# Kernel optimization log

Hardware: AMD Instinct MI355X
Metric: run time of the kernel (lower is better)

## Reference

```python
import jax, jax.numpy as jnp
import numpy as np
from math import comb

K = 10            # Bernstein polynomial order
N = 100000        # num nodes
E = 3200000       # num edges


def _bern_prop(x, row, col, temp):
    """BernNet propagation: sum_k relu(temp)_k * C(K,k)/2^K * L^k (2I-L)^{K-k} x,
    with L = I - D^{-1/2} A D^{-1/2} built from the directed edge list."""
    theta = jax.nn.relu(temp)
    deg = jax.ops.segment_sum(jnp.ones((row.shape[0],), dtype=x.dtype), row, num_segments=N)
    dinv = jnp.where(deg > 0, jax.lax.rsqrt(deg), jnp.zeros_like(deg))
    w = (dinv[row] * dinv[col])[:, None]  # normalized adjacency edge weights [E,1]

    def adj(v):  # A_hat @ v : gather-multiply-scatter over edges
        return jax.ops.segment_sum(v[col] * w, row, num_segments=N)

    # tmp[i] = (2I - L)^i x = (I + A_hat)^i x
    tmp = [x]
    v = x
    for _ in range(K):
        v = v + adj(v)
        tmp.append(v)

    scale = 1.0 / (2 ** K)
    out = (comb(K, 0) * scale) * theta[0] * tmp[K]
    for i in range(K):
        v = tmp[K - i - 1]
        for _ in range(i + 1):  # apply L = I - A_hat, (i+1) times
            v = v - adj(v)
        out = out + (comb(K, i + 1) * scale) * theta[i + 1] * v
    return out


def setup_inputs() -> dict:
    key = jax.random.key(0)
    ks = jax.random.split(key, 5)
    x = jax.random.normal(ks[0], (N, 512), dtype=jnp.float32)
    edge_index = jax.random.randint(ks[1], (2, E), 0, N, dtype=jnp.int32)
    W1 = jax.random.normal(ks[2], (512, 256), dtype=jnp.float32) * 0.04
    b1 = jnp.zeros((256,), jnp.float32)
    W2 = jax.random.normal(ks[3], (256, 64), dtype=jnp.float32) * 0.06
    b2 = jnp.zeros((64,), jnp.float32)
    temp = jnp.ones((K + 1,), jnp.float32)  # Bern_prop param, initialized to ones
    return {"x": x, "edge_index": edge_index, "W1": W1, "b1": b1, "W2": W2, "b2": b2, "temp": temp}


def reference(x, edge_index, W1, b1, W2, b2, temp):
    # eval mode: dropout is identity; self.m (BatchNorm) is never called in forward
    row, col = edge_index[0], edge_index[1]
    h = jax.nn.relu(x @ W1 + b1)   # lin1 + relu
    h = h @ W2 + b2                # lin2 -> [N, num_classes]
    h = _bern_prop(h, row, col, temp)
    return jax.nn.log_softmax(h, axis=1)
```

## Files before the change

kernel.cpp:

```cpp
#include <hip/hip_runtime.h>
#include <hip/hip_bf16.h>

#define K_ORDER 10
#define NNODES  100000
#define NEDGES  3200000

typedef __bf16 bf16x8 __attribute__((ext_vector_type(8)));
typedef float  floatx4 __attribute__((ext_vector_type(4)));

struct WS {
  float* d;
  int*   jmax;
  int*   cnt;
  int*   off;
  int*   cursor;
  float* dinv;
  int*   csr_col;
  float* csr_w;
  short* h1;
  float* h2;
  float* buf0;
  float* buf1;
  short* w1s;
  short* w2s;
};

__device__ inline short f2bf(float f) {
  __hip_bfloat16 h = __float2bfloat16(f);
  return __builtin_bit_cast(short, h);
}

__global__ void k_coeff(const float* __restrict__ temp, WS ws) {
  if (threadIdx.x != 0) return;
  const double C10[11] = {1,10,45,120,210,252,210,120,45,10,1};
  double dd[11];
  for (int j = 0; j <= K_ORDER; ++j) dd[j] = 0.0;
  for (int k = 0; k <= K_ORDER; ++k) {
    double th = temp[k] > 0.f ? (double)temp[k] : 0.0;
    double c  = th * C10[k] / 1024.0;
    double p[11];
    for (int j = 0; j <= K_ORDER; ++j) p[j] = 0.0;
    p[0] = 1.0;
    int deg = 0;
    for (int i = 0; i < K_ORDER - k; ++i) {
      ++deg;
      for (int j = deg; j >= 1; --j) p[j] += p[j-1];
    }
    for (int i = 0; i < k; ++i) {
      ++deg;
      for (int j = deg; j >= 1; --j) p[j] = p[j] - p[j-1];
    }
    for (int j = 0; j <= K_ORDER; ++j) dd[j] += c * p[j];
  }
  int jm = 0;
  for (int j = 1; j <= K_ORDER; ++j) if (dd[j] != 0.0) jm = j;
  for (int j = 0; j <= K_ORDER; ++j) ws.d[j] = (float)dd[j];
  *ws.jmax = jm;
}

__global__ void k_swz(const float* __restrict__ W, short* __restrict__ dst,
                      int Kd, int Nd) {
  int t = blockIdx.x * blockDim.x + threadIdx.x;
  int total = (Kd >> 5) * (Nd >> 4) * 64;
  if (t >= total) return;
  int lane = t & 63, frag = t >> 6;
  int nfr = Nd >> 4;
  int kt = frag / nfr, nc = frag - kt * nfr;
  int m16 = lane & 15, q = lane >> 4;
  int kbase = kt * 32 + q * 8;
  int col = nc * 16 + m16;
  short v[8];
#pragma unroll
  for (int j = 0; j < 8; ++j) v[j] = f2bf(W[(size_t)(kbase + j) * Nd + col]);
  short4* o = (short4*)&dst[(size_t)t * 8];
  o[0] = make_short4(v[0], v[1], v[2], v[3]);
  o[1] = make_short4(v[4], v[5], v[6], v[7]);
}

__global__ __launch_bounds__(256) void k_gemm1(const float* __restrict__ A,
    const short* __restrict__ Bsw, const float* __restrict__ bias,
    short* __restrict__ H1)
{
  __shared__ short As[4 * 64 * 8];
  const int tid = threadIdx.x;
  const int wave = tid >> 6, lane = tid & 63;
  const int q = lane >> 4, m16 = lane & 15;
  const int bm = blockIdx.x * 64;

  const int srow = tid >> 2, kq = tid & 3;
  const int r_ = srow >> 4, m_ = srow & 15;
  int grow = bm + srow; if (grow > NNODES - 1) grow = NNODES - 1;
  const float* aptr = A + (size_t)grow * 512 + kq * 8;
  short* sdst = &As[r_ * 512 + (kq * 16 + m_) * 8];

  float4 p0 = *(const float4*)(aptr);
  float4 p1 = *(const float4*)(aptr + 4);

  floatx4 acc[4][4] = {};

#pragma unroll 1
  for (int kt = 0; kt < 16; ++kt) {
    __syncthreads();
    ((short4*)sdst)[0] = make_short4(f2bf(p0.x), f2bf(p0.y), f2bf(p0.z), f2bf(p0.w));
    ((short4*)sdst)[1] = make_short4(f2bf(p1.x), f2bf(p1.y), f2bf(p1.z), f2bf(p1.w));
    __syncthreads();
    if (kt < 15) {
      p0 = *(const float4*)(aptr + (kt + 1) * 32);
      p1 = *(const float4*)(aptr + (kt + 1) * 32 + 4);
    }
    const short* bbase = Bsw + ((size_t)(kt * 16 + wave * 4) * 64 + lane) * 8;
    bf16x8 bf[4];
#pragma unroll
    for (int c = 0; c < 4; ++c) bf[c] = *(const bf16x8*)(bbase + c * 512);
    bf16x8 af[4];
#pragma unroll
    for (int r = 0; r < 4; ++r) af[r] = *(const bf16x8*)&As[r * 512 + lane * 8];
#pragma unroll
    for (int r = 0; r < 4; ++r)
#pragma unroll
      for (int c = 0; c < 4; ++c)
        acc[r][c] = __builtin_amdgcn_mfma_f32_16x16x32_bf16(af[r], bf[c], acc[r][c], 0, 0, 0);
  }

  float bv[4];
#pragma unroll
  for (int c = 0; c < 4; ++c) bv[c] = bias[wave * 64 + c * 16 + m16];
#pragma unroll
  for (int r = 0; r < 4; ++r) {
    int rb = bm + r * 16 + q * 4;
#pragma unroll
    for (int reg = 0; reg < 4; ++reg) {
      int rowm = rb + reg;
      if (rowm < NNODES) {
        size_t o = (size_t)rowm * 256 + wave * 64 + m16;
#pragma unroll
        for (int c = 0; c < 4; ++c)
          H1[o + c * 16] = f2bf(fmaxf(acc[r][c][reg] + bv[c], 0.f));
      }
    }
  }
}

__global__ __launch_bounds__(256) void k_gemm2(const short* __restrict__ H1,
    const short* __restrict__ B2sw, const float* __restrict__ bias,
    WS ws, float* __restrict__ out)
{
  const int tid = threadIdx.x;
  const int wave = tid >> 6, lane = tid & 63;
  const int q = lane >> 4, m16 = lane & 15;
  const int bm = blockIdx.x * 64;
  int grow = bm + wave * 16 + m16; if (grow > NNODES - 1) grow = NNODES - 1;
  const short* arow = H1 + (size_t)grow * 256 + q * 8;

  floatx4 acc[4] = {};
#pragma unroll
  for (int kt = 0; kt < 8; ++kt) {
    bf16x8 af = *(const bf16x8*)(arow + kt * 32);
    const short* bbase = B2sw + ((size_t)(kt * 4) * 64 + lane) * 8;
#pragma unroll
    for (int c = 0; c < 4; ++c) {
      bf16x8 bf = *(const bf16x8*)(bbase + c * 512);
      acc[c] = __builtin_amdgcn_mfma_f32_16x16x32_bf16(af, bf, acc[c], 0, 0, 0);
    }
  }

  int jm = *ws.jmax;
  float d0 = ws.d[0];
  float bv[4];
#pragma unroll
  for (int c = 0; c < 4; ++c) bv[c] = bias[c * 16 + m16];

  if (jm > 0) {
#pragma unroll
    for (int reg = 0; reg < 4; ++reg) {
      int rowm = bm + wave * 16 + q * 4 + reg;
      if (rowm < NNODES) {
        size_t o = (size_t)rowm * 64 + m16;
#pragma unroll
        for (int c = 0; c < 4; ++c)
          ws.h2[o + c * 16] = acc[c][reg] + bv[c];
      }
    }
  } else {
#pragma unroll
    for (int reg = 0; reg < 4; ++reg) {
      float v[4];
#pragma unroll
      for (int c = 0; c < 4; ++c) v[c] = d0 * (acc[c][reg] + bv[c]);
      float m = fmaxf(fmaxf(v[0], v[1]), fmaxf(v[2], v[3]));
#pragma unroll
      for (int o = 1; o < 16; o <<= 1) m = fmaxf(m, __shfl_xor(m, o));
      float s = 0.f;
#pragma unroll
      for (int c = 0; c < 4; ++c) s += __expf(v[c] - m);
#pragma unroll
      for (int o = 1; o < 16; o <<= 1) s += __shfl_xor(s, o);
      float ls = __logf(s);
      int rowm = bm + wave * 16 + q * 4 + reg;
      if (rowm < NNODES) {
        size_t o = (size_t)rowm * 64 + m16;
#pragma unroll
        for (int c = 0; c < 4; ++c) out[o + c * 16] = v[c] - m - ls;
      }
    }
  }
}

__global__ void k_zero(WS ws) {
  if (*ws.jmax == 0) return;
  int stride = gridDim.x * blockDim.x;
  for (int i = blockIdx.x * blockDim.x + threadIdx.x; i < NNODES; i += stride) {
    ws.cnt[i] = 0; ws.cursor[i] = 0;
  }
}

__global__ void k_count(const int* __restrict__ ei, WS ws) {
  if (*ws.jmax == 0) return;
  int stride = gridDim.x * blockDim.x;
  for (int e = blockIdx.x * blockDim.x + threadIdx.x; e < NEDGES; e += stride)
    atomicAdd(&ws.cnt[ei[e]], 1);
}

__global__ __launch_bounds__(1024) void k_scan(WS ws) {
  if (*ws.jmax == 0) return;
  __shared__ int sdata[1024];
  __shared__ int carry;
  const int t = threadIdx.x;
  if (t == 0) { carry = 0; ws.off[0] = 0; }
  __syncthreads();
  for (int base = 0; base < NNODES; base += 1024) {
    int i = base + t;
    int v = (i < NNODES) ? ws.cnt[i] : 0;
    if (i < NNODES) ws.dinv[i] = v > 0 ? rsqrtf((float)v) : 0.f;
    sdata[t] = v;
    __syncthreads();
    for (int o = 1; o < 1024; o <<= 1) {
      int add = (t >= o) ? sdata[t - o] : 0;
      __syncthreads();
      sdata[t] += add;
      __syncthreads();
    }
    if (i < NNODES) ws.off[i + 1] = carry + sdata[t];
    __syncthreads();
    if (t == 1023) carry += sdata[1023];
    __syncthreads();
  }
}

__global__ void k_scatter(const int* __restrict__ ei, WS ws) {
  if (*ws.jmax == 0) return;
  int stride = gridDim.x * blockDim.x;
  for (int e = blockIdx.x * blockDim.x + threadIdx.x; e < NEDGES; e += stride) {
    int row = ei[e], col = ei[NEDGES + e];
    float wv = ws.dinv[row] * ws.dinv[col];
    int pos = ws.off[row] + atomicAdd(&ws.cursor[row], 1);
    ws.csr_col[pos] = col;
    ws.csr_w[pos]   = wv;
  }
}

__global__ void k_init(WS ws) {
  int jm = *ws.jmax;
  if (jm == 0) return;
  float s = ws.d[jm];
  float* dst = (jm & 1) ? ws.buf1 : ws.buf0;
  int stride = gridDim.x * blockDim.x;
  for (int i = blockIdx.x * blockDim.x + threadIdx.x; i < NNODES * 64; i += stride)
    dst[i] = s * ws.h2[i];
}

__global__ __launch_bounds__(256) void k_adj(WS ws, int j) {
  int jm = *ws.jmax;
  if (j >= jm) return;
  const float* src = ((j + 1) & 1) ? ws.buf1 : ws.buf0;
  float*       dst = (j & 1)       ? ws.buf1 : ws.buf0;
  float dj = ws.d[j];
  int lane = threadIdx.x & 63;
  int wid = blockIdx.x * 4 + (threadIdx.x >> 6);
  int nwaves = gridDim.x * 4;
  for (int node = wid; node < NNODES; node += nwaves) {
    int s = ws.off[node], e = ws.off[node + 1];
    float acc = 0.f;
    for (int base = s; base < e; base += 64) {
      int idx = base + lane;
      int cc = 0; float cw = 0.f;
      if (idx < e) { cc = ws.csr_col[idx]; cw = ws.csr_w[idx]; }
      int n = min(64, e - base);
      for (int t = 0; t < n; ++t) {
        int   c2 = __shfl(cc, t);
        float w2 = __shfl(cw, t);
        acc += w2 * src[(size_t)c2 * 64 + lane];
      }
    }
    dst[(size_t)node * 64 + lane] = acc + dj * ws.h2[(size_t)node * 64 + lane];
  }
}

__global__ __launch_bounds__(256) void k_lsm(WS ws, float* __restrict__ out) {
  if (*ws.jmax == 0) return;
  int wid = blockIdx.x * 4 + (threadIdx.x >> 6);
  if (wid >= NNODES) return;
  int lane = threadIdx.x & 63;
  size_t idx = (size_t)wid * 64 + lane;
  float v = ws.buf0[idx];
  float m = v;
#pragma unroll
  for (int o = 32; o > 0; o >>= 1) m = fmaxf(m, __shfl_xor(m, o));
  float s = __expf(v - m);
#pragma unroll
  for (int o = 32; o > 0; o >>= 1) s += __shfl_xor(s, o);
  out[idx] = (v - m) - __logf(s);
}

extern "C" void kernel_launch(void* const* d_in, const int* in_sizes, int n_in,
                              void* d_out, int out_size, void* d_ws, size_t ws_size,
                              hipStream_t stream) {
  const float* x    = (const float*)d_in[0];
  const int*   ei   = (const int*)  d_in[1];
  const float* W1   = (const float*)d_in[2];
  const float* b1   = (const float*)d_in[3];
  const float* W2   = (const float*)d_in[4];
  const float* b2   = (const float*)d_in[5];
  const float* temp = (const float*)d_in[6];
  float* out = (float*)d_out;

  char* w = (char*)d_ws;
  size_t o = 0;
  auto bump = [&](size_t bytes) { size_t r = o; o += (bytes + 255) & ~(size_t)255; return r; };
  WS ws;
  ws.d       = (float*)(w + bump(11 * 4));
  ws.jmax    = (int*)  (w + bump(4));
  ws.cnt     = (int*)  (w + bump((size_t)NNODES * 4));
  ws.off     = (int*)  (w + bump((size_t)(NNODES + 1) * 4));
  ws.cursor  = (int*)  (w + bump((size_t)NNODES * 4));
  ws.dinv    = (float*)(w + bump((size_t)NNODES * 4));
  ws.csr_col = (int*)  (w + bump((size_t)NEDGES * 4));
  ws.csr_w   = (float*)(w + bump((size_t)NEDGES * 4));
  ws.h1      = (short*)(w + bump((size_t)NNODES * 256 * 2));
  ws.h2      = (float*)(w + bump((size_t)NNODES * 64 * 4));
  ws.buf0    = (float*)(w + bump((size_t)NNODES * 64 * 4));
  ws.buf1    = (float*)(w + bump((size_t)NNODES * 64 * 4));
  ws.w1s     = (short*)(w + bump((size_t)512 * 256 * 2));
  ws.w2s     = (short*)(w + bump((size_t)256 * 64 * 2));

  const int MBLK = (NNODES + 63) / 64;

  k_coeff<<<1, 64, 0, stream>>>(temp, ws);
  k_swz<<<64, 256, 0, stream>>>(W1, ws.w1s, 512, 256);
  k_swz<<<8, 256, 0, stream>>>(W2, ws.w2s, 256, 64);
  k_gemm1<<<MBLK, 256, 0, stream>>>(x, ws.w1s, b1, ws.h1);
  k_gemm2<<<MBLK, 256, 0, stream>>>(ws.h1, ws.w2s, b2, ws, out);
  k_zero   <<<512,  256, 0, stream>>>(ws);
  k_count  <<<1024, 256, 0, stream>>>(ei, ws);
  k_scan   <<<1,   1024, 0, stream>>>(ws);
  k_scatter<<<1024, 256, 0, stream>>>(ei, ws);
  k_init   <<<1024, 256, 0, stream>>>(ws);
  for (int j = K_ORDER - 1; j >= 0; --j)
    k_adj<<<1024, 256, 0, stream>>>(ws, j);
  k_lsm<<<25000, 256, 0, stream>>>(ws, out);
}
```

Measured before the change: 416.4 us.

## Fuse the two GEMMs through shared memory and run graph stages in one cooperative kernel

The two dense layers now run in one kernel: H1 is staged in shared memory instead of round-tripping through global memory. The coefficient computation and weight swizzles merge into a single launch. CSR construction (count, a two-level block scan, scatter), the ten propagation steps and log-softmax all move into one cooperative kernel of 512 blocks with grid syncs in place of separate launches. This removes the H1 traffic and many launch gaps, at the cost of fewer waves (2048 instead of 4096) for the bandwidth-bound gather steps and the overhead of grid-wide barriers.

```diff
diff --git a/kernel.cpp b/kernel.cpp
--- a/kernel.cpp
+++ b/kernel.cpp
@@ -1,5 +1,8 @@
 #include <hip/hip_runtime.h>
 #include <hip/hip_bf16.h>
+#include <hip/hip_cooperative_groups.h>
+
+namespace cg = cooperative_groups;
 
 #define K_ORDER 10
 #define NNODES  100000
@@ -17,12 +20,13 @@
   float* dinv;
   int*   csr_col;
   float* csr_w;
-  short* h1;
   float* h2;
   float* buf0;
   float* buf1;
   short* w1s;
   short* w2s;
+  int*   bsum;
+  int*   bbase;
 };
 
 __device__ inline short f2bf(float f) {
@@ -30,39 +34,8 @@
   return __builtin_bit_cast(short, h);
 }
 
-__global__ void k_coeff(const float* __restrict__ temp, WS ws) {
-  if (threadIdx.x != 0) return;
-  const double C10[11] = {1,10,45,120,210,252,210,120,45,10,1};
-  double dd[11];
-  for (int j = 0; j <= K_ORDER; ++j) dd[j] = 0.0;
-  for (int k = 0; k <= K_ORDER; ++k) {
-    double th = temp[k] > 0.f ? (double)temp[k] : 0.0;
-    double c  = th * C10[k] / 1024.0;
-    double p[11];
-    for (int j = 0; j <= K_ORDER; ++j) p[j] = 0.0;
-    p[0] = 1.0;
-    int deg = 0;
-    for (int i = 0; i < K_ORDER - k; ++i) {
-      ++deg;
-      for (int j = deg; j >= 1; --j) p[j] += p[j-1];
-    }
-    for (int i = 0; i < k; ++i) {
-      ++deg;
-      for (int j = deg; j >= 1; --j) p[j] = p[j] - p[j-1];
-    }
-    for (int j = 0; j <= K_ORDER; ++j) dd[j] += c * p[j];
-  }
-  int jm = 0;
-  for (int j = 1; j <= K_ORDER; ++j) if (dd[j] != 0.0) jm = j;
-  for (int j = 0; j <= K_ORDER; ++j) ws.d[j] = (float)dd[j];
-  *ws.jmax = jm;
-}
-
-__global__ void k_swz(const float* __restrict__ W, short* __restrict__ dst,
-                      int Kd, int Nd) {
-  int t = blockIdx.x * blockDim.x + threadIdx.x;
-  int total = (Kd >> 5) * (Nd >> 4) * 64;
-  if (t >= total) return;
+__device__ inline void swz_body(const float* __restrict__ W, short* __restrict__ dst,
+                                int Kd, int Nd, int t) {
   int lane = t & 63, frag = t >> 6;
   int nfr = Nd >> 4;
   int kt = frag / nfr, nc = frag - kt * nfr;
@@ -77,11 +50,47 @@
   o[1] = make_short4(v[4], v[5], v[6], v[7]);
 }
 
-__global__ __launch_bounds__(256) void k_gemm1(const float* __restrict__ A,
-    const short* __restrict__ Bsw, const float* __restrict__ bias,
-    short* __restrict__ H1)
+__global__ __launch_bounds__(256) void k_swzall(const float* __restrict__ W1,
+    const float* __restrict__ W2, const float* __restrict__ temp, WS ws) {
+  int b = blockIdx.x;
+  if (b < 64) {
+    swz_body(W1, ws.w1s, 512, 256, b * 256 + threadIdx.x);
+  } else if (b < 72) {
+    swz_body(W2, ws.w2s, 256, 64, (b - 64) * 256 + threadIdx.x);
+  } else if (threadIdx.x == 0) {
+    const double C10[11] = {1,10,45,120,210,252,210,120,45,10,1};
+    double dd[11];
+    for (int j = 0; j <= K_ORDER; ++j) dd[j] = 0.0;
+    for (int k = 0; k <= K_ORDER; ++k) {
+      double th = temp[k] > 0.f ? (double)temp[k] : 0.0;
+      double c  = th * C10[k] / 1024.0;
+      double p[11];
+      for (int j = 0; j <= K_ORDER; ++j) p[j] = 0.0;
+      p[0] = 1.0;
+      int deg = 0;
+      for (int i = 0; i < K_ORDER - k; ++i) {
+        ++deg;
+        for (int j = deg; j >= 1; --j) p[j] += p[j-1];
+      }
+      for (int i = 0; i < k; ++i) {
+        ++deg;
+        for (int j = deg; j >= 1; --j) p[j] = p[j] - p[j-1];
+      }
+      for (int j = 0; j <= K_ORDER; ++j) dd[j] += c * p[j];
+    }
+    int jm = 0;
+    for (int j = 1; j <= K_ORDER; ++j) if (dd[j] != 0.0) jm = j;
+    for (int j = 0; j <= K_ORDER; ++j) ws.d[j] = (float)dd[j];
+    *ws.jmax = jm;
+  }
+}
+
+__global__ __launch_bounds__(256) void k_fwd(const float* __restrict__ A,
+    const float* __restrict__ b1, const float* __restrict__ b2,
+    WS ws, float* __restrict__ out)
 {
   __shared__ short As[4 * 64 * 8];
+  __shared__ short H1s[64 * 264];
   const int tid = threadIdx.x;
   const int wave = tid >> 6, lane = tid & 63;
   const int q = lane >> 4, m16 = lane & 15;
@@ -108,7 +117,7 @@
       p0 = *(const float4*)(aptr + (kt + 1) * 32);
       p1 = *(const float4*)(aptr + (kt + 1) * 32 + 4);
     }
-    const short* bbase = Bsw + ((size_t)(kt * 16 + wave * 4) * 64 + lane) * 8;
+    const short* bbase = ws.w1s + ((size_t)(kt * 16 + wave * 4) * 64 + lane) * 8;
     bf16x8 bf[4];
 #pragma unroll
     for (int c = 0; c < 4; ++c) bf[c] = *(const bf16x8*)(bbase + c * 512);
@@ -124,51 +133,35 @@
 
   float bv[4];
 #pragma unroll
-  for (int c = 0; c < 4; ++c) bv[c] = bias[wave * 64 + c * 16 + m16];
-#pragma unroll
-  for (int r = 0; r < 4; ++r) {
-    int rb = bm + r * 16 + q * 4;
-#pragma unroll
-    for (int reg = 0; reg < 4; ++reg) {
-      int rowm = rb + reg;
-      if (rowm < NNODES) {
-        size_t o = (size_t)rowm * 256 + wave * 64 + m16;
-#pragma unroll
-        for (int c = 0; c < 4; ++c)
-          H1[o + c * 16] = f2bf(fmaxf(acc[r][c][reg] + bv[c], 0.f));
-      }
-    }
-  }
-}
-
-__global__ __launch_bounds__(256) void k_gemm2(const short* __restrict__ H1,
-    const short* __restrict__ B2sw, const float* __restrict__ bias,
-    WS ws, float* __restrict__ out)
-{
-  const int tid = threadIdx.x;
-  const int wave = tid >> 6, lane = tid & 63;
-  const int q = lane >> 4, m16 = lane & 15;
-  const int bm = blockIdx.x * 64;
-  int grow = bm + wave * 16 + m16; if (grow > NNODES - 1) grow = NNODES - 1;
-  const short* arow = H1 + (size_t)grow * 256 + q * 8;
-
-  floatx4 acc[4] = {};
+  for (int c = 0; c < 4; ++c) bv[c] = b1[wave * 64 + c * 16 + m16];
+  __syncthreads();
+#pragma unroll
+  for (int r = 0; r < 4; ++r)
+#pragma unroll
+    for (int c = 0; c < 4; ++c)
+#pragma unroll
+      for (int reg = 0; reg < 4; ++reg)
+        H1s[(r * 16 + q * 4 + reg) * 264 + wave * 64 + c * 16 + m16] =
+            f2bf(fmaxf(acc[r][c][reg] + bv[c], 0.f));
+  __syncthreads();
+
+  floatx4 acc2[4] = {};
 #pragma unroll
   for (int kt = 0; kt < 8; ++kt) {
-    bf16x8 af = *(const bf16x8*)(arow + kt * 32);
-    const short* bbase = B2sw + ((size_t)(kt * 4) * 64 + lane) * 8;
+    bf16x8 af2 = *(const bf16x8*)&H1s[(wave * 16 + m16) * 264 + kt * 32 + q * 8];
+    const short* bb = ws.w2s + ((size_t)(kt * 4) * 64 + lane) * 8;
 #pragma unroll
     for (int c = 0; c < 4; ++c) {
-      bf16x8 bf = *(const bf16x8*)(bbase + c * 512);
-      acc[c] = __builtin_amdgcn_mfma_f32_16x16x32_bf16(af, bf, acc[c], 0, 0, 0);
+      bf16x8 bf2 = *(const bf16x8*)(bb + c * 512);
+      acc2[c] = __builtin_amdgcn_mfma_f32_16x16x32_bf16(af2, bf2, acc2[c], 0, 0, 0);
     }
   }
 
   int jm = *ws.jmax;
   float d0 = ws.d[0];
-  float bv[4];
-#pragma unroll
-  for (int c = 0; c < 4; ++c) bv[c] = bias[c * 16 + m16];
+  float bv2[4];
+#pragma unroll
+  for (int c = 0; c < 4; ++c) bv2[c] = b2[c * 16 + m16];
 
   if (jm > 0) {
 #pragma unroll
@@ -178,7 +171,7 @@
         size_t o = (size_t)rowm * 64 + m16;
 #pragma unroll
         for (int c = 0; c < 4; ++c)
-          ws.h2[o + c * 16] = acc[c][reg] + bv[c];
+          ws.h2[o + c * 16] = acc2[c][reg] + bv2[c];
       }
     }
   } else {
@@ -186,7 +179,7 @@
     for (int reg = 0; reg < 4; ++reg) {
       float v[4];
 #pragma unroll
-      for (int c = 0; c < 4; ++c) v[c] = d0 * (acc[c][reg] + bv[c]);
+      for (int c = 0; c < 4; ++c) v[c] = d0 * (acc2[c][reg] + bv2[c]);
       float m = fmaxf(fmaxf(v[0], v[1]), fmaxf(v[2], v[3]));
 #pragma unroll
       for (int o = 1; o < 16; o <<= 1) m = fmaxf(m, __shfl_xor(m, o));
@@ -206,110 +199,107 @@
   }
 }
 
-__global__ void k_zero(WS ws) {
-  if (*ws.jmax == 0) return;
-  int stride = gridDim.x * blockDim.x;
-  for (int i = blockIdx.x * blockDim.x + threadIdx.x; i < NNODES; i += stride) {
-    ws.cnt[i] = 0; ws.cursor[i] = 0;
-  }
-}
-
-__global__ void k_count(const int* __restrict__ ei, WS ws) {
-  if (*ws.jmax == 0) return;
-  int stride = gridDim.x * blockDim.x;
-  for (int e = blockIdx.x * blockDim.x + threadIdx.x; e < NEDGES; e += stride)
-    atomicAdd(&ws.cnt[ei[e]], 1);
-}
-
-__global__ __launch_bounds__(1024) void k_scan(WS ws) {
-  if (*ws.jmax == 0) return;
-  __shared__ int sdata[1024];
-  __shared__ int carry;
+__global__ __launch_bounds__(256) void k_graph(const int* __restrict__ ei,
+                                               WS ws, float* __restrict__ out) {
+  const int jm = *ws.jmax;
+  if (jm == 0) return;
+  cg::grid_group g = cg::this_grid();
   const int t = threadIdx.x;
-  if (t == 0) { carry = 0; ws.off[0] = 0; }
-  __syncthreads();
-  for (int base = 0; base < NNODES; base += 1024) {
-    int i = base + t;
-    int v = (i < NNODES) ? ws.cnt[i] : 0;
-    if (i < NNODES) ws.dinv[i] = v > 0 ? rsqrtf((float)v) : 0.f;
-    sdata[t] = v;
-    __syncthreads();
-    for (int o = 1; o < 1024; o <<= 1) {
-      int add = (t >= o) ? sdata[t - o] : 0;
+  const int gtid = blockIdx.x * 256 + t;
+  const int gstride = 512 * 256;
+
+  for (int i = gtid; i < NNODES; i += gstride) { ws.cnt[i] = 0; ws.cursor[i] = 0; }
+  {
+    float s = ws.d[jm];
+    float* dst = (jm & 1) ? ws.buf1 : ws.buf0;
+    for (int i = gtid; i < NNODES * 64; i += gstride) dst[i] = s * ws.h2[i];
+  }
+  g.sync();
+
+  for (int e = gtid; e < NEDGES; e += gstride) atomicAdd(&ws.cnt[ei[e]], 1);
+  g.sync();
+
+  __shared__ int sd[256];
+  const int i3 = blockIdx.x * 256 + t;
+  {
+    int v = (i3 < NNODES) ? ws.cnt[i3] : 0;
+    if (i3 < NNODES) ws.dinv[i3] = v > 0 ? rsqrtf((float)v) : 0.f;
+    sd[t] = v;
+    __syncthreads();
+    for (int o = 1; o < 256; o <<= 1) {
+      int a = (t >= o) ? sd[t - o] : 0;
       __syncthreads();
-      sdata[t] += add;
+      sd[t] += a;
       __syncthreads();
     }
-    if (i < NNODES) ws.off[i + 1] = carry + sdata[t];
-    __syncthreads();
-    if (t == 1023) carry += sdata[1023];
-    __syncthreads();
-  }
-}
-
-__global__ void k_scatter(const int* __restrict__ ei, WS ws) {
-  if (*ws.jmax == 0) return;
-  int stride = gridDim.x * blockDim.x;
-  for (int e = blockIdx.x * blockDim.x + threadIdx.x; e < NEDGES; e += stride) {
+    if (i3 < NNODES) ws.off[i3 + 1] = sd[t];
+    if (t == 255) ws.bsum[blockIdx.x] = sd[255];
+    if (blockIdx.x == 0 && t == 0) ws.off[0] = 0;
+  }
+  g.sync();
+
+  if (blockIdx.x == 0) {
+    __shared__ int sd2[512];
+    sd2[t] = ws.bsum[t]; sd2[t + 256] = ws.bsum[t + 256];
+    __syncthreads();
+    if (t == 0) {
+      int run = 0;
+      for (int b = 0; b < 512; ++b) { int x = sd2[b]; sd2[b] = run; run += x; }
+    }
+    __syncthreads();
+    ws.bbase[t] = sd2[t]; ws.bbase[t + 256] = sd2[t + 256];
+  }
+  g.sync();
+
+  if (i3 < NNODES) ws.off[i3 + 1] += ws.bbase[blockIdx.x];
+  g.sync();
+
+  for (int e = gtid; e < NEDGES; e += gstride) {
     int row = ei[e], col = ei[NEDGES + e];
     float wv = ws.dinv[row] * ws.dinv[col];
     int pos = ws.off[row] + atomicAdd(&ws.cursor[row], 1);
     ws.csr_col[pos] = col;
     ws.csr_w[pos]   = wv;
   }
-}
-
-__global__ void k_init(WS ws) {
-  int jm = *ws.jmax;
-  if (jm == 0) return;
-  float s = ws.d[jm];
-  float* dst = (jm & 1) ? ws.buf1 : ws.buf0;
-  int stride = gridDim.x * blockDim.x;
-  for (int i = blockIdx.x * blockDim.x + threadIdx.x; i < NNODES * 64; i += stride)
-    dst[i] = s * ws.h2[i];
-}
-
-__global__ __launch_bounds__(256) void k_adj(WS ws, int j) {
-  int jm = *ws.jmax;
-  if (j >= jm) return;
-  const float* src = ((j + 1) & 1) ? ws.buf1 : ws.buf0;
-  float*       dst = (j & 1)       ? ws.buf1 : ws.buf0;
-  float dj = ws.d[j];
-  int lane = threadIdx.x & 63;
-  int wid = blockIdx.x * 4 + (threadIdx.x >> 6);
-  int nwaves = gridDim.x * 4;
-  for (int node = wid; node < NNODES; node += nwaves) {
-    int s = ws.off[node], e = ws.off[node + 1];
-    float acc = 0.f;
-    for (int base = s; base < e; base += 64) {
-      int idx = base + lane;
-      int cc = 0; float cw = 0.f;
-      if (idx < e) { cc = ws.csr_col[idx]; cw = ws.csr_w[idx]; }
-      int n = min(64, e - base);
-      for (int t = 0; t < n; ++t) {
-        int   c2 = __shfl(cc, t);
-        float w2 = __shfl(cw, t);
-        acc += w2 * src[(size_t)c2 * 64 + lane];
-      }
-    }
-    dst[(size_t)node * 64 + lane] = acc + dj * ws.h2[(size_t)node * 64 + lane];
-  }
-}
-
-__global__ __launch_bounds__(256) void k_lsm(WS ws, float* __restrict__ out) {
-  if (*ws.jmax == 0) return;
-  int wid = blockIdx.x * 4 + (threadIdx.x >> 6);
-  if (wid >= NNODES) return;
-  int lane = threadIdx.x & 63;
-  size_t idx = (size_t)wid * 64 + lane;
-  float v = ws.buf0[idx];
-  float m = v;
-#pragma unroll
-  for (int o = 32; o > 0; o >>= 1) m = fmaxf(m, __shfl_xor(m, o));
-  float s = __expf(v - m);
-#pragma unroll
-  for (int o = 32; o > 0; o >>= 1) s += __shfl_xor(s, o);
-  out[idx] = (v - m) - __logf(s);
+  g.sync();
+
+  const int lane = t & 63;
+  const int wid0 = blockIdx.x * 4 + (t >> 6);
+  const int nwaves = 512 * 4;
+  for (int j = jm - 1; j >= 0; --j) {
+    const float* src = ((j + 1) & 1) ? ws.buf1 : ws.buf0;
+    float*       dst = (j & 1)       ? ws.buf1 : ws.buf0;
+    float dj = ws.d[j];
+    for (int node = wid0; node < NNODES; node += nwaves) {
+      int s = ws.off[node], e = ws.off[node + 1];
+      float acc = 0.f;
+      for (int base = s; base < e; base += 64) {
+        int idx = base + lane;
+        int cc = 0; float cw = 0.f;
+        if (idx < e) { cc = ws.csr_col[idx]; cw = ws.csr_w[idx]; }
+        int n = min(64, e - base);
+        for (int u = 0; u < n; ++u) {
+          int   c2 = __shfl(cc, u);
+          float w2 = __shfl(cw, u);
+          acc += w2 * src[(size_t)c2 * 64 + lane];
+        }
+      }
+      dst[(size_t)node * 64 + lane] = acc + dj * ws.h2[(size_t)node * 64 + lane];
+    }
+    g.sync();
+  }
+
+  for (int node = wid0; node < NNODES; node += nwaves) {
+    size_t idx = (size_t)node * 64 + lane;
+    float v = ws.buf0[idx];
+    float m = v;
+#pragma unroll
+    for (int o = 32; o > 0; o >>= 1) m = fmaxf(m, __shfl_xor(m, o));
+    float s = __expf(v - m);
+#pragma unroll
+    for (int o = 32; o > 0; o >>= 1) s += __shfl_xor(s, o);
+    out[idx] = (v - m) - __logf(s);
+  }
 }
 
 extern "C" void kernel_launch(void* const* d_in, const int* in_sizes, int n_in,
@@ -336,26 +326,19 @@
   ws.dinv    = (float*)(w + bump((size_t)NNODES * 4));
   ws.csr_col = (int*)  (w + bump((size_t)NEDGES * 4));
   ws.csr_w   = (float*)(w + bump((size_t)NEDGES * 4));
-  ws.h1      = (short*)(w + bump((size_t)NNODES * 256 * 2));
   ws.h2      = (float*)(w + bump((size_t)NNODES * 64 * 4));
   ws.buf0    = (float*)(w + bump((size_t)NNODES * 64 * 4));
   ws.buf1    = (float*)(w + bump((size_t)NNODES * 64 * 4));
   ws.w1s     = (short*)(w + bump((size_t)512 * 256 * 2));
   ws.w2s     = (short*)(w + bump((size_t)256 * 64 * 2));
+  ws.bsum    = (int*)  (w + bump(512 * 4));
+  ws.bbase   = (int*)  (w + bump(512 * 4));
 
   const int MBLK = (NNODES + 63) / 64;
 
-  k_coeff<<<1, 64, 0, stream>>>(temp, ws);
-  k_swz<<<64, 256, 0, stream>>>(W1, ws.w1s, 512, 256);
-  k_swz<<<8, 256, 0, stream>>>(W2, ws.w2s, 256, 64);
-  k_gemm1<<<MBLK, 256, 0, stream>>>(x, ws.w1s, b1, ws.h1);
-  k_gemm2<<<MBLK, 256, 0, stream>>>(ws.h1, ws.w2s, b2, ws, out);
-  k_zero   <<<512,  256, 0, stream>>>(ws);
-  k_count  <<<1024, 256, 0, stream>>>(ei, ws);
-  k_scan   <<<1,   1024, 0, stream>>>(ws);
-  k_scatter<<<1024, 256, 0, stream>>>(ei, ws);
-  k_init   <<<1024, 256, 0, stream>>>(ws);
-  for (int j = K_ORDER - 1; j >= 0; --j)
-    k_adj<<<1024, 256, 0, stream>>>(ws, j);
-  k_lsm<<<25000, 256, 0, stream>>>(ws, out);
-}
+  k_swzall<<<73, 256, 0, stream>>>(W1, W2, temp, ws);
+  k_fwd<<<MBLK, 256, 0, stream>>>(x, b1, b2, ws, out);
+
+  void* args[] = { (void*)&ei, (void*)&ws, (void*)&out };
+  hipLaunchCooperativeKernel((void*)k_graph, dim3(512), dim3(256), args, 0, stream);
+}
```

New measurement: 391.3 us. 6.0% less time.
